# Optimization experiments

Measured on AMD Instinct MI355X. Metric: run time of the kernel, lower is better.

The kernel has to match this reference:

```python
import jax, jax.numpy as jnp
import numpy as np

EPS = 1e-6

def _norm(x, alpha, beta):
    # torch std is unbiased (n-1); eps added to std (not var)
    d = x.shape[-1]
    mu = jnp.mean(x, axis=-1, keepdims=True)
    xc = x - mu
    std = jnp.sqrt(jnp.sum(xc * xc, axis=-1, keepdims=True) / (d - 1))
    return alpha * xc / (std + EPS) + beta

def setup_inputs() -> dict:
    key = jax.random.key(0)
    B, S, D, P, H, DFF = 4, 2048, 1024, 256, 16, 512
    ks = jax.random.split(key, 24)
    sd = 1.0 / np.sqrt(D)
    inp = {
        "feature_x": jax.random.normal(ks[0], (B, S, D), jnp.float32),
        "param_x": jax.random.normal(ks[1], (B, S, P), jnp.float32),
        "Wq": jax.random.normal(ks[2], (D, D), jnp.float32) * sd,
        "bq": jnp.zeros((D,), jnp.float32),
        "Wk": jax.random.normal(ks[3], (D, D), jnp.float32) * sd,
        "bk": jnp.zeros((D,), jnp.float32),
        "Wv": jax.random.normal(ks[4], (D, D), jnp.float32) * sd,
        "bv": jnp.zeros((D,), jnp.float32),
        "Wo": jax.random.normal(ks[5], (D, D), jnp.float32) * sd,
        "bo": jnp.zeros((D,), jnp.float32),
        "alpha1": jnp.ones((D,), jnp.float32),
        "beta1": jnp.zeros((D,), jnp.float32),
        "alpha2": jnp.ones((D,), jnp.float32),
        "beta2": jnp.zeros((D,), jnp.float32),
        "W1": jax.random.normal(ks[6], (D, DFF), jnp.float32) * sd,
        "b1": jnp.zeros((DFF,), jnp.float32),
        "W2": jax.random.normal(ks[7], (DFF, D), jnp.float32) / np.sqrt(DFF),
        "b2": jnp.zeros((D,), jnp.float32),
        "Wp": jax.random.normal(ks[8], (D + P, P), jnp.float32) / np.sqrt(D + P),
        "bp": jnp.zeros((P,), jnp.float32),
    }
    return inp

def reference(feature_x, param_x, Wq, bq, Wk, bk, Wv, bv, Wo, bo,
              alpha1, beta1, alpha2, beta2, W1, b1, W2, b2, Wp, bp):
    B, S, D = feature_x.shape
    H = 16
    dh = D // H
    # pre-norm (note: original reassigns feature_x = norm_1(feature_x))
    xn = _norm(feature_x, alpha1, beta1)
    q = (xn @ Wq + bq).reshape(B, S, H, dh)
    k = (xn @ Wk + bk).reshape(B, S, H, dh)
    v = (xn @ Wv + bv).reshape(B, S, H, dh)
    scores = jnp.einsum('bqhd,bkhd->bhqk', q, k) / jnp.sqrt(jnp.float32(dh))
    attn = jax.nn.softmax(scores, axis=-1)  # dropout = identity (eval)
    ctx = jnp.einsum('bhqk,bkhd->bqhd', attn, v).reshape(B, S, D)
    attn_out = ctx @ Wo + bo
    x = xn + attn_out
    x2 = _norm(x, alpha2, beta2)
    ff = jax.nn.relu(x2 @ W1 + b1) @ W2 + b2
    x = x + ff
    combined = jnp.concatenate([x, param_x], axis=-1)
    p = combined @ Wp + bp
    return (x, p)
```

## Files before the change

### kernel.cpp

```cpp
#include <hip/hip_runtime.h>
#include <hip/hip_bf16.h>

typedef unsigned short u16;
typedef short short8 __attribute__((ext_vector_type(8)));
typedef float f32x4 __attribute__((ext_vector_type(4)));

#define MELEM 8388608u
__device__ u16 g_ws[(size_t)MELEM * 13];

__device__ __forceinline__ float b2f(u16 u) {
  union { unsigned int i; float f; } v; v.i = ((unsigned int)u) << 16; return v.f;
}
__device__ __forceinline__ u16 f2b(float f) {
  union { float f; unsigned int i; } v; v.f = f;
  return (u16)((v.i + 0x7FFFu + ((v.i >> 16) & 1u)) >> 16);
}
__device__ __forceinline__ unsigned int pk2(float a, float b) {
  union { __hip_bfloat162 h; unsigned int u; } v;
  v.h = __float22bfloat162_rn(make_float2(a, b));
  return v.u;
}
__device__ __forceinline__ f32x4 mfma16(short8 a, short8 b, f32x4 c) {
  return __builtin_amdgcn_mfma_f32_16x16x32_bf16(a, b, c, 0, 0, 0);
}

typedef __attribute__((address_space(3))) unsigned int lds_u32;
typedef const __attribute__((address_space(1))) unsigned int glb_u32;
__device__ __forceinline__ void gld16(u16* l, const u16* g) {
  __builtin_amdgcn_global_load_lds((glb_u32*)g, (lds_u32*)l, 16, 0, 0);
}

#if __has_builtin(__builtin_amdgcn_exp2f)
#define QSCALE 0.18033688011112042f
#define SCLAMP 86.561714f
#define FEXP(x) __builtin_amdgcn_exp2f(x)
#else
#define QSCALE 0.125f
#define SCLAMP 60.0f
#define FEXP(x) __expf(x)
#endif

__device__ __forceinline__ void tr32(const float* __restrict__ W, u16* __restrict__ Wt,
                                     int K, int N, int bx, int by, int tid,
                                     float (*tile)[33]) {
  const int tx = tid & 31, ty = tid >> 5;
#pragma unroll
  for (int i = 0; i < 32; i += 8)
    tile[ty + i][tx] = W[(size_t)(by + ty + i) * N + bx + tx];
  __syncthreads();
#pragma unroll
  for (int i = 0; i < 32; i += 8)
    Wt[(size_t)(bx + ty + i) * K + by + tx] = f2b(tile[tx][ty + i]);
}

__global__ __launch_bounds__(256) void prep_kernel(
    const float* __restrict__ Wq, const float* __restrict__ Wk,
    const float* __restrict__ Wv, const float* __restrict__ Wo,
    const float* __restrict__ W1, const float* __restrict__ W2,
    const float* __restrict__ Wp,
    const float* __restrict__ bq, const float* __restrict__ bk,
    const float* __restrict__ bv, const float* __restrict__ param_x,
    u16* __restrict__ Wqkvt, u16* __restrict__ Wot, u16* __restrict__ W1t,
    u16* __restrict__ W2t, u16* __restrict__ Wpt,
    float* __restrict__ bqkv, u16* __restrict__ px_b) {
  __shared__ float tile[32][33];
  const int bid = blockIdx.x;
  const int tid = threadIdx.x;
  if (bid < 4096) {
    const int j = bid >> 10, r = bid & 1023;
    const int bx = (r & 31) * 32, by = (r >> 5) * 32;
    const float* src = (j == 0) ? Wq : (j == 1) ? Wk : (j == 2) ? Wv : Wo;
    u16* dst = (j == 3) ? Wot : (Wqkvt + (size_t)j * 1024 * 1024);
    tr32(src, dst, 1024, 1024, bx, by, tid, tile);
  } else if (bid < 4608) {
    const int r = bid - 4096;
    tr32(W1, W1t, 1024, 512, (r & 15) * 32, (r >> 4) * 32, tid, tile);
  } else if (bid < 5120) {
    const int r = bid - 4608;
    tr32(W2, W2t, 512, 1024, (r & 31) * 32, (r >> 5) * 32, tid, tile);
  } else if (bid < 5440) {
    const int r = bid - 5120;
    tr32(Wp, Wpt, 1280, 256, (r & 7) * 32, (r >> 3) * 32, tid, tile);
  } else if (bid < 5452) {
    const int i = (bid - 5440) * 256 + tid;
    bqkv[i] = (i < 1024) ? bq[i] : (i < 2048) ? bk[i - 1024] : bv[i - 2048];
  } else {
    const int i = (bid - 5452) * 256 + tid;
    px_b[i] = f2b(param_x[i]);
  }
}

__global__ __launch_bounds__(256) void ln_kernel(const float* __restrict__ x,
                                                 const float* __restrict__ alpha,
                                                 const float* __restrict__ beta,
                                                 u16* __restrict__ outb,
                                                 float* __restrict__ outf) {
  const int D = 1024;
  const int row = blockIdx.x;
  const int tid = threadIdx.x;
  const float4 u = *(const float4*)(x + (size_t)row * D + tid * 4);
  float s1 = u.x + u.y + u.z + u.w;
  float s2 = u.x * u.x + u.y * u.y + u.z * u.z + u.w * u.w;
#pragma unroll
  for (int off = 32; off >= 1; off >>= 1) {
    s1 += __shfl_xor(s1, off, 64);
    s2 += __shfl_xor(s2, off, 64);
  }
  __shared__ float ws1[4], ws2[4];
  if ((tid & 63) == 0) { ws1[tid >> 6] = s1; ws2[tid >> 6] = s2; }
  __syncthreads();
  s1 = ws1[0] + ws1[1] + ws1[2] + ws1[3];
  s2 = ws2[0] + ws2[1] + ws2[2] + ws2[3];
  const float mean = s1 * (1.0f / 1024.0f);
  const float var = fmaxf((s2 - 1024.0f * mean * mean) * (1.0f / 1023.0f), 0.0f);
  const float inv = 1.0f / (sqrtf(var) + 1e-6f);
  const float4 a = *(const float4*)(alpha + tid * 4);
  const float4 b = *(const float4*)(beta + tid * 4);
  const float o0 = a.x * (u.x - mean) * inv + b.x;
  const float o1 = a.y * (u.y - mean) * inv + b.y;
  const float o2 = a.z * (u.z - mean) * inv + b.z;
  const float o3 = a.w * (u.w - mean) * inv + b.w;
  ushort4 ob; ob.x = f2b(o0); ob.y = f2b(o1); ob.z = f2b(o2); ob.w = f2b(o3);
  *(ushort4*)(outb + (size_t)row * D + tid * 4) = ob;
  if (outf) {
    float4 of; of.x = o0; of.y = o1; of.z = o2; of.w = o3;
    *(float4*)(outf + (size_t)row * D + tid * 4) = of;
  }
}

template<int TM, int TN>
__global__ __launch_bounds__(256) void gemm_t(
    const u16* __restrict__ A, const u16* __restrict__ A2,
    const u16* __restrict__ Bt, const float* __restrict__ bias,
    const float* __restrict__ resid, float* __restrict__ Cf, u16* __restrict__ Cb,
    int M, int N, int K, int K1, int relu) {
  __shared__ __align__(16) u16 As[TM * 32];
  __shared__ __align__(16) u16 Bs[TN * 32];
  const int tid = threadIdx.x;
  const int bn = blockIdx.x * TN;
  const int bm = blockIdx.y * TM;
  const int wv = tid >> 6, lane = tid & 63, quad = lane >> 4, l16 = lane & 15;
  constexpr int WN = (TM == 128) ? 64 : TN / 4;
  constexpr int AM = 4, AN = WN / 16;
  const int wm = (TM == 128) ? (wv >> 1) * 64 : 0;
  const int wn = (TM == 128) ? (wv & 1) * 64 : wv * WN;
  const int r0 = tid >> 2;
  const int cc = (tid & 3) * 8;
  f32x4 acc[AM][AN];
#pragma unroll
  for (int i = 0; i < AM; ++i)
#pragma unroll
    for (int j = 0; j < AN; ++j) acc[i][j] = (f32x4){0.f, 0.f, 0.f, 0.f};

  for (int k0 = 0; k0 < K; k0 += 32) {
    const u16* aS; int lda, kk;
    if (A2 != nullptr && k0 >= K1) { aS = A2; lda = K - K1; kk = k0 - K1; }
    else { aS = A; lda = (A2 != nullptr) ? K1 : K; kk = k0; }
#pragma unroll
    for (int i = 0; i < TM / 64; ++i)
      gld16(&As[i * 2048 + tid * 8], aS + (size_t)(bm + i * 64 + r0) * lda + kk + cc);
#pragma unroll
    for (int i = 0; i < TN / 64; ++i)
      gld16(&Bs[i * 2048 + tid * 8], Bt + (size_t)(bn + i * 64 + r0) * K + k0 + cc);
    __syncthreads();
    short8 af[AM], bf[AN];
#pragma unroll
    for (int mi = 0; mi < AM; ++mi)
      af[mi] = *(const short8*)&As[(wm + mi * 16 + l16) * 32 + quad * 8];
#pragma unroll
    for (int ni = 0; ni < AN; ++ni)
      bf[ni] = *(const short8*)&Bs[(wn + ni * 16 + l16) * 32 + quad * 8];
#pragma unroll
    for (int mi = 0; mi < AM; ++mi)
#pragma unroll
      for (int ni = 0; ni < AN; ++ni)
        acc[mi][ni] = mfma16(af[mi], bf[ni], acc[mi][ni]);
    __syncthreads();
  }

#pragma unroll
  for (int ni = 0; ni < AN; ++ni) {
    const int col = bn + wn + ni * 16 + l16;
    const float bb = bias ? bias[col] : 0.0f;
#pragma unroll
    for (int mi = 0; mi < AM; ++mi) {
#pragma unroll
      for (int r = 0; r < 4; ++r) {
        const int row = bm + wm + mi * 16 + quad * 4 + r;
        const size_t off = (size_t)row * N + col;
        float v = acc[mi][ni][r] + bb;
        if (resid) v += resid[off];
        if (relu) v = fmaxf(v, 0.0f);
        if (Cf) Cf[off] = v;
        if (Cb) Cb[off] = f2b(v);
      }
    }
  }
}

__global__ __launch_bounds__(512) void attn_kernel(
    const u16* __restrict__ Q, const u16* __restrict__ Kb,
    const u16* __restrict__ Vb, u16* __restrict__ O, int ldq) {
  const int S = 2048, NT = 32;
  __shared__ __align__(16) u16 Ks[2][64][64];
  __shared__ __align__(16) u16 Vt[2][64][72];
  __shared__ __align__(16) u16 Pb[8][32][40];
  const int tid = threadIdx.x;
  const int swz = ((blockIdx.x & 7) << 6) | (blockIdx.x >> 3);
  const int qt = swz & 7;
  const int bh = swz >> 3;
  const int b = bh >> 4, h = bh & 15;
  const int wv = tid >> 6, lane = tid & 63, quad = lane >> 4, l16 = lane & 15;
  const size_t brow = (size_t)b * S;
  const size_t hoff = (size_t)h * 64;
  const int q0 = qt * 256 + wv * 32;

  short8 qf[2][2];
#pragma unroll
  for (int ni = 0; ni < 2; ++ni)
#pragma unroll
    for (int ks = 0; ks < 2; ++ks) {
      int4 t = *(const int4*)(Q + (brow + q0 + ni * 16 + l16) * ldq + hoff + ks * 32 + quad * 8);
      const u16* p = (const u16*)&t;
      short8 f;
#pragma unroll
      for (int j = 0; j < 8; ++j) f[j] = (short)f2b(b2f(p[j]) * QSCALE);
      qf[ni][ks] = f;
    }

  f32x4 oacc[4][2];
#pragma unroll
  for (int mi = 0; mi < 4; ++mi)
#pragma unroll
    for (int ni = 0; ni < 2; ++ni) oacc[mi][ni] = (f32x4){0.f, 0.f, 0.f, 0.f};
  float lsum[2] = {0.0f, 0.0f};
  const f32x4 z4 = {0.f, 0.f, 0.f, 0.f};

  {
    const int s = tid;
    const int key = s >> 3, c = (s & 7) ^ (key & 7);
    gld16(&Ks[0][0][0] + (size_t)s * 8, Kb + (brow + key) * ldq + hoff + c * 8);
    const int vkey = tid >> 3, c0 = (tid & 7) * 8;
    int4 vv = *(const int4*)(Vb + (brow + vkey) * ldq + hoff + c0);
    const u16* vp = (const u16*)&vv;
    const int rot = tid & 7;
#pragma unroll
    for (int j0 = 0; j0 < 8; ++j0) {
      const int j = (j0 + rot) & 7;
      Vt[0][c0 + j][vkey] = vp[j];
    }
  }
  __syncthreads();

  for (int t = 0; t < NT; ++t) {
    const int p = t & 1, np = p ^ 1;
    int4 va;
    if (t + 1 < NT) {
      const int kbn = (t + 1) * 64;
      const int s = tid;
      const int key = s >> 3, c = (s & 7) ^ (key & 7);
      gld16(&Ks[np][0][0] + (size_t)s * 8, Kb + (brow + kbn + key) * ldq + hoff + c * 8);
      const int vkey = tid >> 3, c0 = (tid & 7) * 8;
      va = *(const int4*)(Vb + (brow + kbn + vkey) * ldq + hoff + c0);
    }

    const u16* ksb = &Ks[p][0][0];
#pragma unroll
    for (int kk = 0; kk < 2; ++kk) {
#pragma unroll
      for (int half = 0; half < 2; ++half) {
        const int m = (kk * 2 + half) * 16 + l16;
        short8 af0 = *(const short8*)(ksb + m * 64 + ((quad ^ (m & 7)) * 8));
        short8 af1 = *(const short8*)(ksb + m * 64 + (((4 + quad) ^ (m & 7)) * 8));
#pragma unroll
        for (int ni = 0; ni < 2; ++ni) {
          f32x4 s = z4;
          s = mfma16(af0, qf[ni][0], s);
          s = mfma16(af1, qf[ni][1], s);
          const float e0 = FEXP(fminf(s[0], SCLAMP));
          const float e1 = FEXP(fminf(s[1], SCLAMP));
          const float e2 = FEXP(fminf(s[2], SCLAMP));
          const float e3 = FEXP(fminf(s[3], SCLAMP));
          lsum[ni] += (e0 + e1) + (e2 + e3);
          uint2 pk;
          pk.x = pk2(e0, e1);
          pk.y = pk2(e2, e3);
          *(uint2*)&Pb[wv][ni * 16 + l16][half * 16 + quad * 4] = pk;
        }
      }
      short8 pf[2];
#pragma unroll
      for (int ni = 0; ni < 2; ++ni)
        pf[ni] = *(const short8*)&Pb[wv][ni * 16 + l16][quad * 8];
      __builtin_amdgcn_s_setprio(1);
#pragma unroll
      for (int mi2 = 0; mi2 < 4; ++mi2) {
        short8 vf = *(const short8*)&Vt[p][mi2 * 16 + l16][kk * 32 + quad * 8];
#pragma unroll
        for (int ni = 0; ni < 2; ++ni)
          oacc[mi2][ni] = mfma16(vf, pf[ni], oacc[mi2][ni]);
      }
      __builtin_amdgcn_s_setprio(0);
    }

    if (t + 1 < NT) {
      const int vkey = tid >> 3, c0 = (tid & 7) * 8;
      const u16* vp = (const u16*)&va;
      const int rot = tid & 7;
#pragma unroll
      for (int j0 = 0; j0 < 8; ++j0) {
        const int j = (j0 + rot) & 7;
        Vt[np][c0 + j][vkey] = vp[j];
      }
      __syncthreads();
    }
  }

#pragma unroll
  for (int ni = 0; ni < 2; ++ni) {
    lsum[ni] += __shfl_xor(lsum[ni], 16, 64);
    lsum[ni] += __shfl_xor(lsum[ni], 32, 64);
  }
#pragma unroll
  for (int ni = 0; ni < 2; ++ni) {
    const float rl = 1.0f / lsum[ni];
    const size_t ob = (brow + q0 + ni * 16 + l16) * 1024 + hoff;
#pragma unroll
    for (int mi2 = 0; mi2 < 4; ++mi2) {
      uint2 ov;
      ov.x = pk2(oacc[mi2][ni][0] * rl, oacc[mi2][ni][1] * rl);
      ov.y = pk2(oacc[mi2][ni][2] * rl, oacc[mi2][ni][3] * rl);
      *(uint2*)(O + ob + mi2 * 16 + quad * 4) = ov;
    }
  }
}

extern "C" void kernel_launch(void* const* d_in, const int* in_sizes, int n_in,
                              void* d_out, int out_size, void* d_ws, size_t ws_size,
                              hipStream_t stream) {
  const int M = 8192, D = 1024, P = 256, DFF = 512;

  const float* feature_x = (const float*)d_in[0];
  const float* param_x   = (const float*)d_in[1];
  const float* Wq = (const float*)d_in[2];  const float* bq = (const float*)d_in[3];
  const float* Wk = (const float*)d_in[4];  const float* bk = (const float*)d_in[5];
  const float* Wv = (const float*)d_in[6];  const float* bv = (const float*)d_in[7];
  const float* Wo = (const float*)d_in[8];  const float* bo = (const float*)d_in[9];
  const float* alpha1 = (const float*)d_in[10]; const float* beta1 = (const float*)d_in[11];
  const float* alpha2 = (const float*)d_in[12]; const float* beta2 = (const float*)d_in[13];
  const float* W1 = (const float*)d_in[14]; const float* b1 = (const float*)d_in[15];
  const float* W2 = (const float*)d_in[16]; const float* b2 = (const float*)d_in[17];
  const float* Wp = (const float*)d_in[18]; const float* bp = (const float*)d_in[19];

  void* sym = nullptr;
  hipGetSymbolAddress(&sym, HIP_SYMBOL(g_ws));
  u16* s = (u16*)sym;

  u16* xn_b   = s + (size_t)MELEM * 0;
  float* xn_f = (float*)(s + (size_t)MELEM * 1);
  u16* qkv_b  = s + (size_t)MELEM * 3;
  u16* ctx    = s + (size_t)MELEM * 6;
  float* x1_f = (float*)(s + (size_t)MELEM * 7);
  u16* x2_b   = s + (size_t)MELEM * 9;
  u16* h1_b   = s + (size_t)MELEM * 10;
  u16* xcp_b  = s + (size_t)MELEM * 11;
  u16* wreg   = s + (size_t)MELEM * 12;
  u16* px_b   = wreg;
  u16* Wqkvt  = px_b + 2097152;
  u16* Wot    = Wqkvt + 3145728;
  u16* W1t    = Wot + 1048576;
  u16* W2t    = W1t + 524288;
  u16* Wpt    = W2t + 524288;
  float* bqkv = (float*)(Wpt + 327680);

  float* xout_f = (float*)d_out;
  float* pout_f = xout_f + (size_t)M * D;

  dim3 blk(256);
  prep_kernel<<<13644, blk, 0, stream>>>(Wq, Wk, Wv, Wo, W1, W2, Wp, bq, bk, bv,
                                         param_x, Wqkvt, Wot, W1t, W2t, Wpt,
                                         bqkv, px_b);

  ln_kernel<<<M, blk, 0, stream>>>(feature_x, alpha1, beta1, xn_b, xn_f);
  gemm_t<128, 128><<<dim3(24, 64), blk, 0, stream>>>(xn_b, nullptr, Wqkvt, bqkv, nullptr,
                                                     nullptr, qkv_b, M, 3072, D, D, 0);
  attn_kernel<<<512, dim3(512), 0, stream>>>(qkv_b, qkv_b + 1024, qkv_b + 2048, ctx, 3072);
  gemm_t<128, 128><<<dim3(8, 64), blk, 0, stream>>>(ctx, nullptr, Wot, bo, xn_f,
                                                    x1_f, nullptr, M, D, D, D, 0);
  ln_kernel<<<M, blk, 0, stream>>>(x1_f, alpha2, beta2, x2_b, nullptr);
  gemm_t<64, 128><<<dim3(4, 128), blk, 0, stream>>>(x2_b, nullptr, W1t, b1, nullptr,
                                                    nullptr, h1_b, M, DFF, D, D, 1);
  gemm_t<128, 128><<<dim3(8, 64), blk, 0, stream>>>(h1_b, nullptr, W2t, b2, x1_f,
                                                    xout_f, xcp_b, M, D, DFF, DFF, 0);
  gemm_t<64, 64><<<dim3(4, 128), blk, 0, stream>>>(xcp_b, px_b, Wpt, bp, nullptr,
                                                   pout_f, nullptr, M, P, D + P, D, 0);
}
```

Before: 565.1 us.

## Write V transposed from QKV GEMM epilogue and async-load it in attention

The QKV projection epilogue now writes the V third of its output directly in a per-(batch, head-dim) transposed layout into a separate buffer, and Q/K are stored with a reduced 2048 row stride. The attention kernel then loads V tiles with the same asynchronous swizzled global-to-LDS copy used for K, removing the register-staged scalar transpose into LDS and the padded Vt buffer. This cuts LDS write traffic and VGPR pressure in attention, at the cost of strided 8-byte global stores in the GEMM epilogue for V columns.

```diff
diff --git a/kernel.cpp b/kernel.cpp
--- a/kernel.cpp
+++ b/kernel.cpp
@@ -133,7 +133,8 @@
     const u16* __restrict__ A, const u16* __restrict__ A2,
     const u16* __restrict__ Bt, const float* __restrict__ bias,
     const float* __restrict__ resid, float* __restrict__ Cf, u16* __restrict__ Cb,
-    int M, int N, int K, int K1, int relu) {
+    u16* __restrict__ Vt_out,
+    int M, int N, int K, int K1, int relu, int ldcb) {
   __shared__ __align__(16) u16 As[TM * 32];
   __shared__ __align__(16) u16 Bs[TN * 32];
   const int tid = threadIdx.x;
@@ -184,15 +185,27 @@
     const float bb = bias ? bias[col] : 0.0f;
 #pragma unroll
     for (int mi = 0; mi < AM; ++mi) {
-#pragma unroll
-      for (int r = 0; r < 4; ++r) {
-        const int row = bm + wm + mi * 16 + quad * 4 + r;
-        const size_t off = (size_t)row * N + col;
-        float v = acc[mi][ni][r] + bb;
-        if (resid) v += resid[off];
-        if (relu) v = fmaxf(v, 0.0f);
-        if (Cf) Cf[off] = v;
-        if (Cb) Cb[off] = f2b(v);
+      if (Vt_out != nullptr && col >= 2048) {
+        const int s0 = bm + wm + mi * 16 + quad * 4;
+        const int bb_idx = s0 >> 11;
+        const size_t voff = ((size_t)(bb_idx * 1024 + col - 2048) << 11) + (s0 & 2047);
+        ushort4 w;
+        w.x = f2b(acc[mi][ni][0] + bb);
+        w.y = f2b(acc[mi][ni][1] + bb);
+        w.z = f2b(acc[mi][ni][2] + bb);
+        w.w = f2b(acc[mi][ni][3] + bb);
+        *(ushort4*)(Vt_out + voff) = w;
+      } else {
+#pragma unroll
+        for (int r = 0; r < 4; ++r) {
+          const int row = bm + wm + mi * 16 + quad * 4 + r;
+          const size_t off = (size_t)row * N + col;
+          float v = acc[mi][ni][r] + bb;
+          if (resid) v += resid[off];
+          if (relu) v = fmaxf(v, 0.0f);
+          if (Cf) Cf[off] = v;
+          if (Cb) Cb[(size_t)row * ldcb + col] = f2b(v);
+        }
       }
     }
   }
@@ -200,10 +213,10 @@
 
 __global__ __launch_bounds__(512) void attn_kernel(
     const u16* __restrict__ Q, const u16* __restrict__ Kb,
-    const u16* __restrict__ Vb, u16* __restrict__ O, int ldq) {
+    const u16* __restrict__ Vtg, u16* __restrict__ O, int ldq) {
   const int S = 2048, NT = 32;
   __shared__ __align__(16) u16 Ks[2][64][64];
-  __shared__ __align__(16) u16 Vt[2][64][72];
+  __shared__ __align__(16) u16 Vs[2][64][64];
   __shared__ __align__(16) u16 Pb[8][32][40];
   const int tid = threadIdx.x;
   const int swz = ((blockIdx.x & 7) << 6) | (blockIdx.x >> 3);
@@ -214,6 +227,7 @@
   const size_t brow = (size_t)b * S;
   const size_t hoff = (size_t)h * 64;
   const int q0 = qt * 256 + wv * 32;
+  const u16* Vg = Vtg + (((size_t)(b * 1024 + h * 64)) << 11);
 
   short8 qf[2][2];
 #pragma unroll
@@ -236,35 +250,23 @@
   float lsum[2] = {0.0f, 0.0f};
   const f32x4 z4 = {0.f, 0.f, 0.f, 0.f};
 
-  {
-    const int s = tid;
-    const int key = s >> 3, c = (s & 7) ^ (key & 7);
-    gld16(&Ks[0][0][0] + (size_t)s * 8, Kb + (brow + key) * ldq + hoff + c * 8);
-    const int vkey = tid >> 3, c0 = (tid & 7) * 8;
-    int4 vv = *(const int4*)(Vb + (brow + vkey) * ldq + hoff + c0);
-    const u16* vp = (const u16*)&vv;
-    const int rot = tid & 7;
-#pragma unroll
-    for (int j0 = 0; j0 < 8; ++j0) {
-      const int j = (j0 + rot) & 7;
-      Vt[0][c0 + j][vkey] = vp[j];
-    }
-  }
+  const int srow = tid >> 3;
+  const int sc = (tid & 7) ^ (srow & 7);
+
+  gld16(&Ks[0][0][0] + (size_t)tid * 8, Kb + (brow + srow) * ldq + hoff + sc * 8);
+  gld16(&Vs[0][0][0] + (size_t)tid * 8, Vg + ((size_t)srow << 11) + sc * 8);
   __syncthreads();
 
   for (int t = 0; t < NT; ++t) {
     const int p = t & 1, np = p ^ 1;
-    int4 va;
     if (t + 1 < NT) {
       const int kbn = (t + 1) * 64;
-      const int s = tid;
-      const int key = s >> 3, c = (s & 7) ^ (key & 7);
-      gld16(&Ks[np][0][0] + (size_t)s * 8, Kb + (brow + kbn + key) * ldq + hoff + c * 8);
-      const int vkey = tid >> 3, c0 = (tid & 7) * 8;
-      va = *(const int4*)(Vb + (brow + kbn + vkey) * ldq + hoff + c0);
+      gld16(&Ks[np][0][0] + (size_t)tid * 8, Kb + (brow + kbn + srow) * ldq + hoff + sc * 8);
+      gld16(&Vs[np][0][0] + (size_t)tid * 8, Vg + ((size_t)srow << 11) + kbn + sc * 8);
     }
 
     const u16* ksb = &Ks[p][0][0];
+    const u16* vsb = &Vs[p][0][0];
 #pragma unroll
     for (int kk = 0; kk < 2; ++kk) {
 #pragma unroll
@@ -295,7 +297,8 @@
       __builtin_amdgcn_s_setprio(1);
 #pragma unroll
       for (int mi2 = 0; mi2 < 4; ++mi2) {
-        short8 vf = *(const short8*)&Vt[p][mi2 * 16 + l16][kk * 32 + quad * 8];
+        const int dh = mi2 * 16 + l16;
+        short8 vf = *(const short8*)(vsb + dh * 64 + (((kk * 4 + quad) ^ (dh & 7)) * 8));
 #pragma unroll
         for (int ni = 0; ni < 2; ++ni)
           oacc[mi2][ni] = mfma16(vf, pf[ni], oacc[mi2][ni]);
@@ -303,17 +306,7 @@
       __builtin_amdgcn_s_setprio(0);
     }
 
-    if (t + 1 < NT) {
-      const int vkey = tid >> 3, c0 = (tid & 7) * 8;
-      const u16* vp = (const u16*)&va;
-      const int rot = tid & 7;
-#pragma unroll
-      for (int j0 = 0; j0 < 8; ++j0) {
-        const int j = (j0 + rot) & 7;
-        Vt[np][c0 + j][vkey] = vp[j];
-      }
-      __syncthreads();
-    }
+    if (t + 1 < NT) __syncthreads();
   }
 
 #pragma unroll
@@ -359,6 +352,7 @@
   u16* xn_b   = s + (size_t)MELEM * 0;
   float* xn_f = (float*)(s + (size_t)MELEM * 1);
   u16* qkv_b  = s + (size_t)MELEM * 3;
+  u16* vt     = s + (size_t)MELEM * 5;
   u16* ctx    = s + (size_t)MELEM * 6;
   float* x1_f = (float*)(s + (size_t)MELEM * 7);
   u16* x2_b   = s + (size_t)MELEM * 9;
@@ -383,15 +377,20 @@
 
   ln_kernel<<<M, blk, 0, stream>>>(feature_x, alpha1, beta1, xn_b, xn_f);
   gemm_t<128, 128><<<dim3(24, 64), blk, 0, stream>>>(xn_b, nullptr, Wqkvt, bqkv, nullptr,
-                                                     nullptr, qkv_b, M, 3072, D, D, 0);
-  attn_kernel<<<512, dim3(512), 0, stream>>>(qkv_b, qkv_b + 1024, qkv_b + 2048, ctx, 3072);
+                                                     nullptr, qkv_b, vt,
+                                                     M, 3072, D, D, 0, 2048);
+  attn_kernel<<<512, dim3(512), 0, stream>>>(qkv_b, qkv_b + 1024, vt, ctx, 2048);
   gemm_t<128, 128><<<dim3(8, 64), blk, 0, stream>>>(ctx, nullptr, Wot, bo, xn_f,
-                                                    x1_f, nullptr, M, D, D, D, 0);
+                                                    x1_f, nullptr, nullptr,
+                                                    M, D, D, D, 0, D);
   ln_kernel<<<M, blk, 0, stream>>>(x1_f, alpha2, beta2, x2_b, nullptr);
   gemm_t<64, 128><<<dim3(4, 128), blk, 0, stream>>>(x2_b, nullptr, W1t, b1, nullptr,
-                                                    nullptr, h1_b, M, DFF, D, D, 1);
+                                                    nullptr, h1_b, nullptr,
+                                                    M, DFF, D, D, 1, DFF);
   gemm_t<128, 128><<<dim3(8, 64), blk, 0, stream>>>(h1_b, nullptr, W2t, b2, x1_f,
-                                                    xout_f, xcp_b, M, D, DFF, DFF, 0);
+                                                    xout_f, xcp_b, nullptr,
+                                                    M, D, DFF, DFF, 0, D);
   gemm_t<64, 64><<<dim3(4, 128), blk, 0, stream>>>(xcp_b, px_b, Wpt, bp, nullptr,
-                                                   pout_f, nullptr, M, P, D + P, D, 0);
-}
+                                                   pout_f, nullptr, nullptr,
+                                                   M, P, D + P, D, 0, P);
+}
```

Result: faster. 539.0 us (-4.6%).
